# Kernel optimization log

Hardware: AMD Instinct MI355X
Metric: run time of the kernel (lower is better)

The kernel has to match this reference:

```python
import jax, jax.numpy as jnp
import numpy as np

NUM_HEADS = 12

def setup_inputs() -> dict:
    key = jax.random.key(0)
    k1, k2, k3 = jax.random.split(key, 3)
    B, N, D = 16, 1024, 768
    x = jax.random.normal(k1, (B, N, D), dtype=jnp.float32)
    w_qkv = jax.random.normal(k2, (D, 3 * D), dtype=jnp.float32) * (D ** -0.5)
    b_qkv = jnp.zeros((3 * D,), dtype=jnp.float32)
    w_proj = jax.random.normal(k3, (D, D), dtype=jnp.float32) * (D ** -0.5)
    b_proj = jnp.zeros((D,), dtype=jnp.float32)
    return {"x": x, "w_qkv": w_qkv, "b_qkv": b_qkv, "w_proj": w_proj, "b_proj": b_proj}

def reference(x, w_qkv, b_qkv, w_proj, b_proj):
    B, N, D = x.shape
    H = NUM_HEADS
    Hd = D // H
    scale = Hd ** -0.5
    qkv = x @ w_qkv + b_qkv                       # (B, N, 3D)
    qkv = qkv.reshape(B, N, 3, H, Hd)
    q, k, v = qkv[:, :, 0], qkv[:, :, 1], qkv[:, :, 2]  # (B, N, H, Hd)
    attn = jnp.einsum('bnhd,bmhd->bhnm', q, k) * scale  # (B, H, N, N)
    attn = jax.nn.softmax(attn, axis=-1)
    out = jnp.einsum('bhnm,bmhd->bnhd', attn, v).reshape(B, N, D)
    return out @ w_proj + b_proj
```

## Files before the change

kernel.cpp:

```cpp
#include <hip/hip_runtime.h>


typedef _Float16 half8 __attribute__((ext_vector_type(8)));
typedef _Float16 half4 __attribute__((ext_vector_type(4)));
typedef __fp16   fp16x2 __attribute__((ext_vector_type(2)));
typedef float    f32x4  __attribute__((ext_vector_type(4)));
typedef float    f32x16 __attribute__((ext_vector_type(16)));
typedef unsigned int u32x4 __attribute__((ext_vector_type(4)));

#define DI __device__ __forceinline__

constexpr int   BATCH  = 16;
constexpr int   SEQ    = 1024;
constexpr int   DM     = 768;
constexpr int   NH     = 12;
constexpr int   HD     = 64;
constexpr float SCALE  = 0.125f;
constexpr float LOG2E  = 1.4426950408889634f;

DI void copy16(_Float16* dst, const _Float16* src) {
  *(u32x4*)dst = *(const u32x4*)src;
}

DI int pack_rtz(float a, float b) {
  union { fp16x2 h; int i; } u;
  u.h = __builtin_amdgcn_cvt_pkrtz(a, b);
  return u.i;
}

DI void gld16(const _Float16* g, _Float16* l) {
  __builtin_amdgcn_global_load_lds(
      (const __attribute__((address_space(1))) void*)g,
      (__attribute__((address_space(3))) void*)l, 16, 0, 0);
}

__global__ void cvt_wt2_kernel(const float* __restrict__ wq,
                               _Float16* __restrict__ wqT,
                               const float* __restrict__ wp,
                               _Float16* __restrict__ wpT) {
  __shared__ float tile[32][33];
  const int by = blockIdx.y;
  const float* w; _Float16* wt; int N, nb;
  if (by < 72) { w = wq; wt = wqT; N = 2304; nb = by * 32; }
  else         { w = wp; wt = wpT; N = 768;  nb = (by - 72) * 32; }
  const int K = 768;
  int kb = blockIdx.x * 32;
  int tx = threadIdx.x & 31, ty = threadIdx.x >> 5;
#pragma unroll
  for (int i = 0; i < 32; i += 8)
    tile[ty + i][tx] = w[(size_t)(kb + ty + i) * N + nb + tx];
  __syncthreads();
#pragma unroll
  for (int i = 0; i < 32; i += 8)
    wt[(size_t)(nb + ty + i) * K + kb + tx] = (_Float16)tile[tx][ty + i];
}

__launch_bounds__(512, 3)
__global__ void gemm_qkv_kernel(const float* __restrict__ X,
                                const _Float16* __restrict__ Bt,
                                const float* __restrict__ bias,
                                _Float16* __restrict__ Qo,
                                _Float16* __restrict__ Ko,
                                _Float16* __restrict__ VTo) {
  __shared__ _Float16 sh[24576];
  _Float16* Cs = sh;
  const int tid  = threadIdx.x;
  const int lin  = blockIdx.x;
  const int xcd  = lin & 7, j = lin >> 3;
  const int ct   = j % 9;
  const int m0   = ((j / 9) * 8 + xcd) * 128;
  const int n0   = ct * 256;
  const int w    = tid >> 6, lane = tid & 63;
  const int quad = lane >> 4, l15 = lane & 15;
  const int wr   = w >> 2, wc = w & 3;

  f32x4 acc[4][4] = {};

  const int rA = tid >> 2, sA = tid & 3;
  const float* gaA = X + (size_t)(m0 + rA) * 768 + sA * 8;
  const int so = rA * 32 + sA * 8;

  const _Float16* gbB = Bt + (size_t)(n0 + ((w * 128 + lane) >> 2)) * 768
                           + (lane & 3) * 8;
  const int ldst = w * 1024;

  auto CVT_WRITE = [&](float4 a0, float4 a1, _Float16* As) {
    half8 h0;
    h0[0] = (_Float16)a0.x; h0[1] = (_Float16)a0.y;
    h0[2] = (_Float16)a0.z; h0[3] = (_Float16)a0.w;
    h0[4] = (_Float16)a1.x; h0[5] = (_Float16)a1.y;
    h0[6] = (_Float16)a1.z; h0[7] = (_Float16)a1.w;
    *(half8*)(As + so) = h0;
  };

  {
    float4 a0 = *(const float4*)(gaA);
    float4 a1 = *(const float4*)(gaA + 4);
    CVT_WRITE(a0, a1, sh);
    gld16(gbB,            sh + 4096 + ldst);
    gld16(gbB + 16 * 768, sh + 4096 + ldst + 512);
  }

  for (int kt = 0; kt < 24; ++kt) {
    __syncthreads();
    float4 a0, a1;
    if (kt < 23) {
      const int k0 = (kt + 1) * 32;
      a0 = *(const float4*)(gaA + k0);
      a1 = *(const float4*)(gaA + k0 + 4);
      _Float16* Bsn = sh + ((kt + 1) & 1) * 12288 + 4096;
      gld16(gbB + k0,            Bsn + ldst);
      gld16(gbB + k0 + 16 * 768, Bsn + ldst + 512);
    }

    const _Float16* As = sh + (kt & 1) * 12288;
    const _Float16* Bs = As + 4096;

    half8 af[4], bf[4];
#pragma unroll
    for (int mi = 0; mi < 4; mi++)
      af[mi] = *(const half8*)&As[(wr * 64 + mi * 16 + l15) * 32 + quad * 8];
#pragma unroll
    for (int ni = 0; ni < 4; ni++)
      bf[ni] = *(const half8*)&Bs[(wc * 64 + ni * 16 + l15) * 32 + quad * 8];
#pragma unroll
    for (int mi = 0; mi < 4; mi++)
#pragma unroll
      for (int ni = 0; ni < 4; ni++)
        acc[mi][ni] = __builtin_amdgcn_mfma_f32_16x16x32_f16(
            af[mi], bf[ni], acc[mi][ni], 0, 0, 0);

    if (kt < 23)
      CVT_WRITE(a0, a1, sh + ((kt + 1) & 1) * 12288);
  }
  __syncthreads();

  const int   sec    = ct / 3;
  const int   h0     = (ct % 3) * 4;
  const float oscale = (sec == 0) ? SCALE : 1.0f;
  float bcol[4];
#pragma unroll
  for (int ni = 0; ni < 4; ni++)
    bcol[ni] = bias[n0 + wc * 64 + ni * 16 + l15];

  const int b     = m0 >> 10;
  const int nrow0 = m0 & 1023;

#pragma unroll
  for (int p = 0; p < 2; ++p) {
    if (p) __syncthreads();
    if (wr == p) {
#pragma unroll
      for (int mi = 0; mi < 4; mi++)
#pragma unroll
        for (int ni = 0; ni < 4; ni++) {
          int col = wc * 64 + ni * 16 + l15;
          int row = mi * 16 + quad * 4;
#pragma unroll
          for (int r = 0; r < 4; r++)
            Cs[(row + r) * 264 + col] =
                (_Float16)((acc[mi][ni][r] + bcol[ni]) * oscale);
        }
    }
    __syncthreads();

    if (sec < 2) {
      _Float16* dst = (sec == 0) ? Qo : Ko;
      int row = tid >> 3, seg = tid & 7;
      int hl = seg >> 1, off32 = (seg & 1) * 32;
      _Float16* g = dst +
          ((size_t)((b * NH + h0 + hl) * SEQ + nrow0 + p * 64 + row)) * HD + off32;
      const _Float16* s = &Cs[row * 264 + hl * 64 + off32];
      copy16(g, s);
      copy16(g + 8, s + 8);
      copy16(g + 16, s + 16);
      copy16(g + 24, s + 24);
    } else {
      int c = tid & 255, rh = tid >> 8;
      int hl = c >> 6, d = c & 63;
      _Float16 tmp[32];
#pragma unroll
      for (int jj = 0; jj < 32; jj++) tmp[jj] = Cs[(rh * 32 + jj) * 264 + c];
      _Float16* g = VTo + ((size_t)((b * NH + h0 + hl) * HD + d)) * SEQ
                        + nrow0 + p * 64 + rh * 32;
#pragma unroll
      for (int jj = 0; jj < 4; jj++)
        copy16(g + jj * 8, (const _Float16*)&tmp[jj * 8]);
    }
  }
}

__launch_bounds__(256, 2)
__global__ void attn_kernel(const _Float16* __restrict__ Q,
                            const _Float16* __restrict__ K,
                            const _Float16* __restrict__ VT,
                            _Float16* __restrict__ Oh) {
  __shared__ _Float16 smem[2][2][64 * 72];
  _Float16* OLds = &smem[0][0][0];

  const int tid = threadIdx.x;
  const int i   = blockIdx.x;
  const int bh  = (i & 7) * 24 + ((i >> 3) >> 2);
  const int q0  = ((i >> 3) & 3) * 256;
  const int b   = bh / NH, hh = bh - b * NH;
  const int w   = tid >> 6, lane = tid & 63;
  const int l31 = lane & 31, h = lane >> 5;

  const _Float16* Qg = Q  + (size_t)bh * SEQ * HD;
  const _Float16* Kg = K  + (size_t)bh * SEQ * HD;
  const _Float16* Vg = VT + (size_t)bh * HD * SEQ;

  half8 qb[2][4];
#pragma unroll
  for (int N = 0; N < 2; N++) {
    const _Float16* qrow = Qg + (size_t)(q0 + w * 64 + N * 32 + l31) * HD + h * 8;
#pragma unroll
    for (int s = 0; s < 4; s++)
      qb[N][s] = *(const half8*)(qrow + s * 16);
  }

  const int  sr  = (tid & 127) >> 1;
  const int  sp  = tid & 1;
  const bool isK = tid < 128;
  const _Float16* sg = isK ? (Kg + sr * HD + sp * 32)
                           : (Vg + (size_t)sr * SEQ + sp * 32);
  const int sstep = isK ? 64 * HD : 64;
  const int soff  = (isK ? 0 : 64 * 72) + sr * 72 + sp * 32;

  u32x4 pf[4];
#pragma unroll
  for (int c = 0; c < 4; c++) pf[c] = *(const u32x4*)(sg + c * 8);
#pragma unroll
  for (int c = 0; c < 4; c++) *(u32x4*)(&smem[0][0][0] + soff + c * 8) = pf[c];

  f32x16 of[2][2];
#pragma unroll
  for (int D = 0; D < 2; D++)
#pragma unroll
    for (int N = 0; N < 2; N++)
#pragma unroll
      for (int r = 0; r < 16; r++) of[D][N][r] = 0.f;
  float m_[2] = {-1e30f, -1e30f}, l_[2] = {0.f, 0.f};

  for (int kt = 0; kt < 16; ++kt) {
    if (kt < 15) {
      const _Float16* nsg = sg + (kt + 1) * sstep;
#pragma unroll
      for (int c = 0; c < 4; c++) pf[c] = *(const u32x4*)(nsg + c * 8);
    }
    __syncthreads();
    const _Float16* Ks = &smem[kt & 1][0][0];
    const _Float16* Vs = &smem[kt & 1][1][0];

    f32x16 sf[2][2];
#pragma unroll
    for (int M = 0; M < 2; M++)
#pragma unroll
      for (int N = 0; N < 2; N++)
#pragma unroll
        for (int r = 0; r < 16; r++) sf[M][N][r] = 0.f;
#pragma unroll
    for (int s = 0; s < 4; s++) {
      half8 ka0 = *(const half8*)&Ks[l31 * 72 + s * 16 + h * 8];
      half8 ka1 = *(const half8*)&Ks[(32 + l31) * 72 + s * 16 + h * 8];
#pragma unroll
      for (int N = 0; N < 2; N++) {
        sf[0][N] = __builtin_amdgcn_mfma_f32_32x32x16_f16(ka0, qb[N][s], sf[0][N], 0, 0, 0);
        sf[1][N] = __builtin_amdgcn_mfma_f32_32x32x16_f16(ka1, qb[N][s], sf[1][N], 0, 0, 0);
      }
    }

    float alpha[2], c1[2], tsum[2];
#pragma unroll
    for (int N = 0; N < 2; N++) {
      float tmax = -1e30f;
#pragma unroll
      for (int r = 0; r < 16; r++)
        tmax = fmaxf(tmax, fmaxf(sf[0][N][r], sf[1][N][r]));
      tmax = fmaxf(tmax, __shfl_xor(tmax, 32, 64));
      float mnew = fmaxf(m_[N], tmax);
      alpha[N] = __builtin_amdgcn_exp2f((m_[N] - mnew) * LOG2E);
      m_[N] = mnew;
      c1[N] = mnew * LOG2E;
      tsum[N] = 0.f;
    }

    int pdw[2][2][8];
#pragma unroll
    for (int M = 0; M < 2; M++)
#pragma unroll
      for (int N = 0; N < 2; N++) {
#pragma unroll
        for (int r = 0; r < 16; r++) {
          float p = __builtin_amdgcn_exp2f(sf[M][N][r] * LOG2E - c1[N]);
          sf[M][N][r] = p;
          tsum[N] += p;
        }
#pragma unroll
        for (int u = 0; u < 8; u++)
          pdw[M][N][u] = pack_rtz(sf[M][N][2 * u], sf[M][N][2 * u + 1]);
      }
#pragma unroll
    for (int N = 0; N < 2; N++) {
      tsum[N] += __shfl_xor(tsum[N], 32, 64);
      l_[N] = l_[N] * alpha[N] + tsum[N];
    }
#pragma unroll
    for (int D = 0; D < 2; D++)
#pragma unroll
      for (int N = 0; N < 2; N++)
#pragma unroll
        for (int r = 0; r < 16; r++) of[D][N][r] *= alpha[N];

#pragma unroll
    for (int t = 0; t < 4; ++t) {
      const int M = t >> 1, s2 = (t & 1) * 4;
      half8 va0 = *(const half8*)&Vs[l31 * 72 + t * 16 + h * 8];
      half8 va1 = *(const half8*)&Vs[(32 + l31) * 72 + t * 16 + h * 8];
#pragma unroll
      for (int N = 0; N < 2; N++) {
        int a0 = pdw[M][N][s2 + 0], a1 = pdw[M][N][s2 + 1];
        int a2 = pdw[M][N][s2 + 2], a3 = pdw[M][N][s2 + 3];
        int e0 = h ? a0 : a2, e1 = h ? a1 : a3;
        int r0 = __shfl_xor(e0, 32, 64), r1 = __shfl_xor(e1, 32, 64);
        union { u32x4 u; half8 hv; } bb;
        bb.u[0] = h ? r0 : a0; bb.u[1] = h ? r1 : a1;
        bb.u[2] = h ? a2 : r0; bb.u[3] = h ? a3 : r1;
        of[0][N] = __builtin_amdgcn_mfma_f32_32x32x16_f16(va0, bb.hv, of[0][N], 0, 0, 0);
        of[1][N] = __builtin_amdgcn_mfma_f32_32x32x16_f16(va1, bb.hv, of[1][N], 0, 0, 0);
      }
    }

    if (kt < 15) {
      _Float16* dst = &smem[(kt + 1) & 1][0][0] + soff;
#pragma unroll
      for (int c = 0; c < 4; c++) *(u32x4*)(dst + c * 8) = pf[c];
    }
  }

  __syncthreads();
  float inv[2] = {1.0f / l_[0], 1.0f / l_[1]};
  int* OW = (int*)OLds;
#pragma unroll
  for (int N = 0; N < 2; N++) {
    const int q_local = w * 64 + N * 32 + l31;
#pragma unroll
    for (int D = 0; D < 2; D++)
#pragma unroll
      for (int u = 0; u < 8; u++) {
        int v = pack_rtz(of[D][N][2 * u] * inv[N], of[D][N][2 * u + 1] * inv[N]);
        int dwi = 16 * D + 4 * (u >> 1) + (u & 1) + 2 * h;
        OW[q_local * 36 + dwi] = v;
      }
  }
  __syncthreads();
#pragma unroll
  for (int p = 0; p < 8; p++) {
    int q = p * 32 + (tid >> 3), c = tid & 7;
    *(u32x4*)(Oh + (size_t)(b * SEQ + q0 + q) * DM + hh * HD + c * 8) =
        *(const u32x4*)&OLds[q * 72 + c * 8];
  }
}

__launch_bounds__(512, 3)
__global__ void gemm_proj_kernel(const _Float16* __restrict__ A,
                                 const _Float16* __restrict__ Bt,
                                 const float* __restrict__ bias,
                                 float* __restrict__ out) {
  __shared__ _Float16 sh[24576];
  const int tid  = threadIdx.x;
  const int lin  = blockIdx.x;
  const int xcd  = lin & 7, j = lin >> 3;
  const int ct   = j % 3;
  const int m0   = ((j / 3) * 8 + xcd) * 128;
  const int n0   = ct * 256;
  const int w    = tid >> 6, lane = tid & 63;
  const int quad = lane >> 4, l15 = lane & 15;
  const int wr   = w >> 2, wc = w & 3;

  f32x4 acc[4][4] = {};

  const _Float16* gaA = A + (size_t)(m0 + ((w * 64 + lane) >> 2)) * 768
                          + (lane & 3) * 8;
  const int ldstA = w * 512;
  const _Float16* gbB = Bt + (size_t)(n0 + ((w * 128 + lane) >> 2)) * 768
                           + (lane & 3) * 8;
  const int ldstB = w * 1024;

  auto STAGE = [&](int buf, int kt) {
    _Float16* As = sh + buf * 12288;
    _Float16* Bs = As + 4096;
    const _Float16* a = gaA + kt * 32;
    const _Float16* b = gbB + kt * 32;
    gld16(a,            As + ldstA);
    gld16(b,            Bs + ldstB);
    gld16(b + 16 * 768, Bs + ldstB + 512);
  };

  STAGE(0, 0);

  for (int kt = 0; kt < 24; ++kt) {
    __syncthreads();
    if (kt < 23) STAGE((kt + 1) & 1, kt + 1);

    const _Float16* As = sh + (kt & 1) * 12288;
    const _Float16* Bs = As + 4096;

    half8 af[4], bf[4];
#pragma unroll
    for (int mi = 0; mi < 4; mi++)
      af[mi] = *(const half8*)&As[(wr * 64 + mi * 16 + l15) * 32 + quad * 8];
#pragma unroll
    for (int ni = 0; ni < 4; ni++)
      bf[ni] = *(const half8*)&Bs[(wc * 64 + ni * 16 + l15) * 32 + quad * 8];
#pragma unroll
    for (int mi = 0; mi < 4; mi++)
#pragma unroll
      for (int ni = 0; ni < 4; ni++)
        acc[mi][ni] = __builtin_amdgcn_mfma_f32_16x16x32_f16(
            af[mi], bf[ni], acc[mi][ni], 0, 0, 0);
  }

  float bcol[4];
#pragma unroll
  for (int ni = 0; ni < 4; ni++)
    bcol[ni] = bias[n0 + wc * 64 + ni * 16 + l15];
#pragma unroll
  for (int mi = 0; mi < 4; mi++)
#pragma unroll
    for (int ni = 0; ni < 4; ni++) {
      int col = n0 + wc * 64 + ni * 16 + l15;
      int row = m0 + wr * 64 + mi * 16 + quad * 4;
#pragma unroll
      for (int r = 0; r < 4; r++)
        out[(size_t)(row + r) * 768 + col] = acc[mi][ni][r] + bcol[ni];
    }
}

extern "C" void kernel_launch(void* const* d_in, const int* in_sizes, int n_in,
                              void* d_out, int out_size, void* d_ws, size_t ws_size,
                              hipStream_t stream) {
  const float* x      = (const float*)d_in[0];
  const float* w_qkv  = (const float*)d_in[1];
  const float* b_qkv  = (const float*)d_in[2];
  const float* w_proj = (const float*)d_in[3];
  const float* b_proj = (const float*)d_in[4];
  float* out = (float*)d_out;

  char* ws = (char*)d_ws;
  _Float16* wqkvT  = (_Float16*)(ws);
  _Float16* wprojT = (_Float16*)(ws + 3538944);
  _Float16* Qp     = (_Float16*)(ws + 4718592);
  _Float16* Kp     = (_Float16*)(ws + 29884416);
  _Float16* VTp    = (_Float16*)(ws + 55050240);
  _Float16* Ohp    = (_Float16*)(ws + 80216064);

  cvt_wt2_kernel<<<dim3(24, 96), 256, 0, stream>>>(w_qkv, wqkvT, w_proj, wprojT);
  gemm_qkv_kernel<<<dim3(1152), 512, 0, stream>>>(x, wqkvT, b_qkv, Qp, Kp, VTp);
  attn_kernel<<<dim3(768), 256, 0, stream>>>(Qp, Kp, VTp, Ohp);
  gemm_proj_kernel<<<dim3(384), 512, 0, stream>>>(Ohp, wprojT, b_proj, out);
}
```

Baseline: 299.4 us.

## Halve attention query tile, use direct global-to-LDS loads with XOR swizzle

The attention kernel now gives each wave 32 query rows instead of 64, so the grid doubles to 1536 blocks and the launch bound allows three blocks per CU. K/V staging moves from register prefetch plus LDS store to a gld16 direct-to-LDS copy issued right after the barrier. Padded 72-wide LDS rows are replaced by unpadded 64-wide rows with an XOR swizzle to avoid bank conflicts. This cuts register pressure and the LDS footprint to raise occupancy, but each K/V tile is now reused by half as many queries, doubling K/V traffic into LDS.

```diff
diff --git a/kernel.cpp b/kernel.cpp
--- a/kernel.cpp
+++ b/kernel.cpp
@@ -190,18 +190,19 @@
   }
 }
 
-__launch_bounds__(256, 2)
+__launch_bounds__(256, 3)
 __global__ void attn_kernel(const _Float16* __restrict__ Q,
                             const _Float16* __restrict__ K,
                             const _Float16* __restrict__ VT,
                             _Float16* __restrict__ Oh) {
-  __shared__ _Float16 smem[2][2][64 * 72];
+  __shared__ _Float16 smem[2][2][4096];
   _Float16* OLds = &smem[0][0][0];
 
   const int tid = threadIdx.x;
   const int i   = blockIdx.x;
-  const int bh  = (i & 7) * 24 + ((i >> 3) >> 2);
-  const int q0  = ((i >> 3) & 3) * 256;
+  const int xcd = i & 7, j = i >> 3;
+  const int bh  = xcd * 24 + (j >> 3);
+  const int q0  = (j & 7) * 128;
   const int b   = bh / NH, hh = bh - b * NH;
   const int w   = tid >> 6, lane = tid & 63;
   const int l31 = lane & 31, h = lane >> 5;
@@ -210,155 +211,123 @@
   const _Float16* Kg = K  + (size_t)bh * SEQ * HD;
   const _Float16* Vg = VT + (size_t)bh * HD * SEQ;
 
-  half8 qb[2][4];
-#pragma unroll
-  for (int N = 0; N < 2; N++) {
-    const _Float16* qrow = Qg + (size_t)(q0 + w * 64 + N * 32 + l31) * HD + h * 8;
-#pragma unroll
-    for (int s = 0; s < 4; s++)
-      qb[N][s] = *(const half8*)(qrow + s * 16);
-  }
-
-  const int  sr  = (tid & 127) >> 1;
-  const int  sp  = tid & 1;
-  const bool isK = tid < 128;
-  const _Float16* sg = isK ? (Kg + sr * HD + sp * 32)
-                           : (Vg + (size_t)sr * SEQ + sp * 32);
-  const int sstep = isK ? 64 * HD : 64;
-  const int soff  = (isK ? 0 : 64 * 72) + sr * 72 + sp * 32;
-
-  u32x4 pf[4];
-#pragma unroll
-  for (int c = 0; c < 4; c++) pf[c] = *(const u32x4*)(sg + c * 8);
-#pragma unroll
-  for (int c = 0; c < 4; c++) *(u32x4*)(&smem[0][0][0] + soff + c * 8) = pf[c];
-
-  f32x16 of[2][2];
+  half8 qb[4];
+  {
+    const _Float16* qrow = Qg + (size_t)(q0 + w * 32 + l31) * HD + h * 8;
+#pragma unroll
+    for (int s = 0; s < 4; s++) qb[s] = *(const half8*)(qrow + s * 16);
+  }
+
+  const int rS  = tid >> 3;
+  const int csw = ((lane & 7) ^ (lane >> 3)) << 3;
+  const _Float16* srcK = Kg + rS * HD + csw;
+  const _Float16* srcV = Vg + (size_t)rS * SEQ + csw;
+
+  auto STAGE = [&](int buf, int kt) {
+    _Float16* base = &smem[0][0][0] + buf * 8192;
+#pragma unroll
+    for (int c = 0; c < 2; c++) {
+      gld16(srcK + (kt * 64 + c * 32) * HD, base + c * 2048 + w * 512);
+      gld16(srcV + kt * 64 + c * 32 * SEQ, base + 4096 + c * 2048 + w * 512);
+    }
+  };
+
+  f32x16 of[2];
 #pragma unroll
   for (int D = 0; D < 2; D++)
 #pragma unroll
-    for (int N = 0; N < 2; N++)
-#pragma unroll
-      for (int r = 0; r < 16; r++) of[D][N][r] = 0.f;
-  float m_[2] = {-1e30f, -1e30f}, l_[2] = {0.f, 0.f};
+    for (int r = 0; r < 16; r++) of[D][r] = 0.f;
+  float m_ = -1e30f, l_ = 0.f;
+
+  const int cs0 = (l31 & 7) << 3;
+
+  STAGE(0, 0);
 
   for (int kt = 0; kt < 16; ++kt) {
-    if (kt < 15) {
-      const _Float16* nsg = sg + (kt + 1) * sstep;
-#pragma unroll
-      for (int c = 0; c < 4; c++) pf[c] = *(const u32x4*)(nsg + c * 8);
-    }
     __syncthreads();
+    if (kt < 15) STAGE((kt + 1) & 1, kt + 1);
     const _Float16* Ks = &smem[kt & 1][0][0];
     const _Float16* Vs = &smem[kt & 1][1][0];
 
-    f32x16 sf[2][2];
-#pragma unroll
-    for (int M = 0; M < 2; M++)
-#pragma unroll
-      for (int N = 0; N < 2; N++)
-#pragma unroll
-        for (int r = 0; r < 16; r++) sf[M][N][r] = 0.f;
+    f32x16 sf[2];
+#pragma unroll
+    for (int r = 0; r < 16; r++) { sf[0][r] = 0.f; sf[1][r] = 0.f; }
 #pragma unroll
     for (int s = 0; s < 4; s++) {
-      half8 ka0 = *(const half8*)&Ks[l31 * 72 + s * 16 + h * 8];
-      half8 ka1 = *(const half8*)&Ks[(32 + l31) * 72 + s * 16 + h * 8];
-#pragma unroll
-      for (int N = 0; N < 2; N++) {
-        sf[0][N] = __builtin_amdgcn_mfma_f32_32x32x16_f16(ka0, qb[N][s], sf[0][N], 0, 0, 0);
-        sf[1][N] = __builtin_amdgcn_mfma_f32_32x32x16_f16(ka1, qb[N][s], sf[1][N], 0, 0, 0);
+      const int cc = (s * 16 + h * 8) ^ cs0;
+      half8 ka0 = *(const half8*)&Ks[l31 * 64 + cc];
+      half8 ka1 = *(const half8*)&Ks[(32 + l31) * 64 + cc];
+      sf[0] = __builtin_amdgcn_mfma_f32_32x32x16_f16(ka0, qb[s], sf[0], 0, 0, 0);
+      sf[1] = __builtin_amdgcn_mfma_f32_32x32x16_f16(ka1, qb[s], sf[1], 0, 0, 0);
+    }
+
+    float tmax = -1e30f;
+#pragma unroll
+    for (int r = 0; r < 16; r++)
+      tmax = fmaxf(tmax, fmaxf(sf[0][r], sf[1][r]));
+    tmax = fmaxf(tmax, __shfl_xor(tmax, 32, 64));
+    float mnew  = fmaxf(m_, tmax);
+    float alpha = __builtin_amdgcn_exp2f((m_ - mnew) * LOG2E);
+    m_ = mnew;
+    float c1 = mnew * LOG2E, tsum = 0.f;
+
+    int pdw[2][8];
+#pragma unroll
+    for (int M = 0; M < 2; M++) {
+#pragma unroll
+      for (int r = 0; r < 16; r++) {
+        float p = __builtin_amdgcn_exp2f(sf[M][r] * LOG2E - c1);
+        sf[M][r] = p;
+        tsum += p;
       }
-    }
-
-    float alpha[2], c1[2], tsum[2];
-#pragma unroll
-    for (int N = 0; N < 2; N++) {
-      float tmax = -1e30f;
-#pragma unroll
-      for (int r = 0; r < 16; r++)
-        tmax = fmaxf(tmax, fmaxf(sf[0][N][r], sf[1][N][r]));
-      tmax = fmaxf(tmax, __shfl_xor(tmax, 32, 64));
-      float mnew = fmaxf(m_[N], tmax);
-      alpha[N] = __builtin_amdgcn_exp2f((m_[N] - mnew) * LOG2E);
-      m_[N] = mnew;
-      c1[N] = mnew * LOG2E;
-      tsum[N] = 0.f;
-    }
-
-    int pdw[2][2][8];
-#pragma unroll
-    for (int M = 0; M < 2; M++)
-#pragma unroll
-      for (int N = 0; N < 2; N++) {
-#pragma unroll
-        for (int r = 0; r < 16; r++) {
-          float p = __builtin_amdgcn_exp2f(sf[M][N][r] * LOG2E - c1[N]);
-          sf[M][N][r] = p;
-          tsum[N] += p;
-        }
-#pragma unroll
-        for (int u = 0; u < 8; u++)
-          pdw[M][N][u] = pack_rtz(sf[M][N][2 * u], sf[M][N][2 * u + 1]);
-      }
-#pragma unroll
-    for (int N = 0; N < 2; N++) {
-      tsum[N] += __shfl_xor(tsum[N], 32, 64);
-      l_[N] = l_[N] * alpha[N] + tsum[N];
-    }
+#pragma unroll
+      for (int u = 0; u < 8; u++)
+        pdw[M][u] = pack_rtz(sf[M][2 * u], sf[M][2 * u + 1]);
+    }
+    tsum += __shfl_xor(tsum, 32, 64);
+    l_ = l_ * alpha + tsum;
 #pragma unroll
     for (int D = 0; D < 2; D++)
 #pragma unroll
-      for (int N = 0; N < 2; N++)
-#pragma unroll
-        for (int r = 0; r < 16; r++) of[D][N][r] *= alpha[N];
+      for (int r = 0; r < 16; r++) of[D][r] *= alpha;
 
 #pragma unroll
     for (int t = 0; t < 4; ++t) {
       const int M = t >> 1, s2 = (t & 1) * 4;
-      half8 va0 = *(const half8*)&Vs[l31 * 72 + t * 16 + h * 8];
-      half8 va1 = *(const half8*)&Vs[(32 + l31) * 72 + t * 16 + h * 8];
-#pragma unroll
-      for (int N = 0; N < 2; N++) {
-        int a0 = pdw[M][N][s2 + 0], a1 = pdw[M][N][s2 + 1];
-        int a2 = pdw[M][N][s2 + 2], a3 = pdw[M][N][s2 + 3];
-        int e0 = h ? a0 : a2, e1 = h ? a1 : a3;
-        int r0 = __shfl_xor(e0, 32, 64), r1 = __shfl_xor(e1, 32, 64);
-        union { u32x4 u; half8 hv; } bb;
-        bb.u[0] = h ? r0 : a0; bb.u[1] = h ? r1 : a1;
-        bb.u[2] = h ? a2 : r0; bb.u[3] = h ? a3 : r1;
-        of[0][N] = __builtin_amdgcn_mfma_f32_32x32x16_f16(va0, bb.hv, of[0][N], 0, 0, 0);
-        of[1][N] = __builtin_amdgcn_mfma_f32_32x32x16_f16(va1, bb.hv, of[1][N], 0, 0, 0);
-      }
-    }
-
-    if (kt < 15) {
-      _Float16* dst = &smem[(kt + 1) & 1][0][0] + soff;
-#pragma unroll
-      for (int c = 0; c < 4; c++) *(u32x4*)(dst + c * 8) = pf[c];
+      const int cc = (t * 16 + h * 8) ^ cs0;
+      half8 va0 = *(const half8*)&Vs[l31 * 64 + cc];
+      half8 va1 = *(const half8*)&Vs[(32 + l31) * 64 + cc];
+      int a0 = pdw[M][s2 + 0], a1 = pdw[M][s2 + 1];
+      int a2 = pdw[M][s2 + 2], a3 = pdw[M][s2 + 3];
+      int e0 = h ? a0 : a2, e1 = h ? a1 : a3;
+      int r0 = __shfl_xor(e0, 32, 64), r1 = __shfl_xor(e1, 32, 64);
+      union { u32x4 u; half8 hv; } bb;
+      bb.u[0] = h ? r0 : a0; bb.u[1] = h ? r1 : a1;
+      bb.u[2] = h ? a2 : r0; bb.u[3] = h ? a3 : r1;
+      of[0] = __builtin_amdgcn_mfma_f32_32x32x16_f16(va0, bb.hv, of[0], 0, 0, 0);
+      of[1] = __builtin_amdgcn_mfma_f32_32x32x16_f16(va1, bb.hv, of[1], 0, 0, 0);
     }
   }
 
   __syncthreads();
-  float inv[2] = {1.0f / l_[0], 1.0f / l_[1]};
+  float inv = 1.0f / l_;
   int* OW = (int*)OLds;
-#pragma unroll
-  for (int N = 0; N < 2; N++) {
-    const int q_local = w * 64 + N * 32 + l31;
-#pragma unroll
-    for (int D = 0; D < 2; D++)
-#pragma unroll
-      for (int u = 0; u < 8; u++) {
-        int v = pack_rtz(of[D][N][2 * u] * inv[N], of[D][N][2 * u + 1] * inv[N]);
-        int dwi = 16 * D + 4 * (u >> 1) + (u & 1) + 2 * h;
-        OW[q_local * 36 + dwi] = v;
-      }
-  }
+  const int q_local = w * 32 + l31;
+  const int qs = (q_local & 7) << 2;
+#pragma unroll
+  for (int D = 0; D < 2; D++)
+#pragma unroll
+    for (int u = 0; u < 8; u++) {
+      int v = pack_rtz(of[D][2 * u] * inv, of[D][2 * u + 1] * inv);
+      int dwi = 16 * D + 4 * (u >> 1) + (u & 1) + 2 * h;
+      OW[q_local * 32 + (dwi ^ qs)] = v;
+    }
   __syncthreads();
 #pragma unroll
-  for (int p = 0; p < 8; p++) {
+  for (int p = 0; p < 4; p++) {
     int q = p * 32 + (tid >> 3), c = tid & 7;
     *(u32x4*)(Oh + (size_t)(b * SEQ + q0 + q) * DM + hh * HD + c * 8) =
-        *(const u32x4*)&OLds[q * 72 + c * 8];
+        *(const u32x4*)&OLds[q * 64 + ((c ^ (q & 7)) * 8)];
   }
 }
 
@@ -457,6 +426,6 @@
 
   cvt_wt2_kernel<<<dim3(24, 96), 256, 0, stream>>>(w_qkv, wqkvT, w_proj, wprojT);
   gemm_qkv_kernel<<<dim3(1152), 512, 0, stream>>>(x, wqkvT, b_qkv, Qp, Kp, VTp);
-  attn_kernel<<<dim3(768), 256, 0, stream>>>(Qp, Kp, VTp, Ohp);
+  attn_kernel<<<dim3(1536), 256, 0, stream>>>(Qp, Kp, VTp, Ohp);
   gemm_proj_kernel<<<dim3(384), 512, 0, stream>>>(Ohp, wprojT, b_proj, out);
 }
```

Result: slower. 308.6 us (+3.1%).
